# Kernel tuning notes

Measured on AMD Instinct MI355X. Metric: run time of the kernel, lower is better.

Reference implementation:

```python
import jax, jax.numpy as jnp
import numpy as np

S, B, I, H, O = 1024, 64, 512, 2048, 512


def setup_inputs() -> dict:
    key = jax.random.key(0)
    k1, k2, k3, k4, k5 = jax.random.split(key, 5)
    X = jax.random.normal(k1, (S, B, I), dtype=jnp.float32)
    W_ih = jax.random.normal(k2, (H, I), dtype=jnp.float32) * (1.0 / np.sqrt(I))
    hh = jax.random.uniform(k3, (H,), dtype=jnp.float32)  # clamped-to-[-1,1] diagonal recurrence
    W_ho = jax.random.normal(k4, (O, H), dtype=jnp.float32) * (1.0 / np.sqrt(H))
    b_ho = jax.random.normal(k5, (O,), dtype=jnp.float32) * 0.01
    return {"X": X, "W_ih": W_ih, "hh": hh, "W_ho": W_ho, "b_ho": b_ho}


def reference(X, W_ih, hh, W_ho, b_ho):
    # Batch the input->hidden projection over the whole sequence in one GEMM:
    # u[s,b,h] = X[s,b,i] @ W_ih[h,i]^T
    u = jnp.einsum('sbi,hi->sbh', X, W_ih)
    h0 = jnp.zeros((X.shape[1], W_ih.shape[0]), dtype=X.dtype)

    def step(h, u_t):
        h_new = jnp.abs(u_t + hh * h)
        return h_new, None

    h_final, _ = jax.lax.scan(step, h0, u)
    Y = h_final @ W_ho.T + b_ho  # [B, O]
    return Y
```

## Files before the change

kernel.cpp:

```cpp
#include <hip/hip_runtime.h>
#include <hip/hip_bf16.h>
#include <stdint.h>

#define S_LEN 1024
#define B_SZ  64
#define I_SZ  512
#define H_SZ  2048
#define O_SZ  512
#define BH    (B_SZ * H_SZ)

typedef __bf16  bf16x8 __attribute__((ext_vector_type(8)));
typedef float   f32x4  __attribute__((ext_vector_type(4)));

static __device__ __forceinline__ ushort f2bf(float f) {
  union { float f; unsigned u; } v; v.f = f;
  unsigned r = v.u + 0x7FFFu + ((v.u >> 16) & 1u);
  return (ushort)(r >> 16);
}

#define GLOAD_LDS16(gp, lp) \
  __builtin_amdgcn_global_load_lds( \
      (__attribute__((address_space(1))) void*)(gp), \
      (__attribute__((address_space(3))) void*)(lp), 16, 0, 0)

__global__ __launch_bounds__(256) void convert_f32_bf16_kernel(
    const float4* __restrict__ in, ushort4* __restrict__ out, int n4) {
  int i = blockIdx.x * 256 + threadIdx.x;
  if (i >= n4) return;
  float4 v = in[i];
  ushort4 o; o.x = f2bf(v.x); o.y = f2bf(v.y); o.z = f2bf(v.z); o.w = f2bf(v.w);
  out[i] = o;
}

__global__ __launch_bounds__(256, 2) void gemm_u_kernel(
    const ushort* __restrict__ A, const ushort* __restrict__ Bm,
    ushort* __restrict__ U) {
  __shared__ __align__(16) ushort smem[17408];
  ushort* As = smem;
  ushort* Bs = smem + 8192;

  const int tid  = threadIdx.x;
  const int wave = tid >> 6;
  const int lane = tid & 63;

  const int b  = blockIdx.x;
  const int x  = b & 7;
  const int j  = b >> 3;
  const int bn = j & 15;
  const int bm = ((j >> 4) << 3) | x;

  const int wm = (wave >> 1) * 64;
  const int wn = (wave & 1) * 64;
  const int ml = lane & 15;
  const int q  = lane >> 4;

  f32x4 acc[4][4] = {};

  const int r0     = wave * 32;
  const int srow   = lane >> 3;
  const int schunk = ((lane & 7) - srow) & 7;
  const ushort* gA = A  + (size_t)(bm * 128 + r0 + srow) * I_SZ + schunk * 8;
  const ushort* gB = Bm + (size_t)(bn * 128 + r0 + srow) * I_SZ + schunk * 8;
  ushort* lA = As + r0 * 64;
  ushort* lB = Bs + r0 * 64;

  int swz[2];
  swz[0] = ((q + ml) & 7) * 8;
  swz[1] = ((4 + q + ml) & 7) * 8;
  int arow[4], brow[4];
  #pragma unroll
  for (int i = 0; i < 4; ++i) {
    arow[i] = (wm + i * 16 + ml) * 64;
    brow[i] = (wn + i * 16 + ml) * 64;
  }

  for (int kt = 0; kt < I_SZ / 64; ++kt) {
    __syncthreads();
    #pragma unroll
    for (int jj = 0; jj < 4; ++jj) {
      GLOAD_LDS16(gA + (size_t)(jj * 8) * I_SZ + kt * 64, lA + jj * 512);
      GLOAD_LDS16(gB + (size_t)(jj * 8) * I_SZ + kt * 64, lB + jj * 512);
    }
    __syncthreads();
    #pragma unroll
    for (int ks = 0; ks < 2; ++ks) {
      bf16x8 af[4], bfr[4];
      #pragma unroll
      for (int i = 0; i < 4; ++i) {
        af[i]  = *(const bf16x8*)&As[arow[i] + swz[ks]];
        bfr[i] = *(const bf16x8*)&Bs[brow[i] + swz[ks]];
      }
      #pragma unroll
      for (int mi = 0; mi < 4; ++mi)
        #pragma unroll
        for (int ni = 0; ni < 4; ++ni)
          acc[mi][ni] = __builtin_amdgcn_mfma_f32_16x16x32_bf16(
              af[mi], bfr[ni], acc[mi][ni], 0, 0, 0);
    }
  }

  __syncthreads();
  ushort* Cs = smem;
  const int rl0 = wm + q * 4;
  #pragma unroll
  for (int mi = 0; mi < 4; ++mi)
    #pragma unroll
    for (int ni = 0; ni < 4; ++ni)
      #pragma unroll
      for (int r = 0; r < 4; ++r)
        Cs[(rl0 + mi * 16 + r) * 136 + wn + ni * 16 + ml] = f2bf(acc[mi][ni][r]);
  __syncthreads();

  const size_t gbase = (size_t)(bm * 128) * H_SZ + bn * 128;
  #pragma unroll
  for (int i = 0; i < 8; ++i) {
    int chunk = i * 256 + tid;
    int row = chunk >> 4, c8 = chunk & 15;
    uint4 v = *(const uint4*)&Cs[row * 136 + c8 * 8];
    *(uint4*)&U[gbase + (size_t)row * H_SZ + c8 * 8] = v;
  }
}

__global__ __launch_bounds__(256) void scan_kernel(
    const uint* __restrict__ U2, const float* __restrict__ hh,
    float* __restrict__ hstate) {
  int p = blockIdx.x * 256 + threadIdx.x;
  int h0 = (2 * p) & (H_SZ - 1);
  float c0 = hh[h0], c1 = hh[h0 + 1];
  float ha = 0.0f, hb = 0.0f;
  const uint* Up = U2 + p;
  for (int s0 = 0; s0 < S_LEN; s0 += 16) {
    uint v[16];
    #pragma unroll
    for (int t = 0; t < 16; ++t) v[t] = Up[(size_t)(s0 + t) * (BH / 2)];
    #pragma unroll
    for (int t = 0; t < 16; ++t) {
      float ua = __builtin_bit_cast(float, (v[t] & 0xffffu) << 16);
      float ub = __builtin_bit_cast(float, v[t] & 0xffff0000u);
      ha = fabsf(ua + c0 * ha);
      hb = fabsf(ub + c1 * hb);
    }
  }
  ((float2*)hstate)[p] = make_float2(ha, hb);
}

__global__ __launch_bounds__(256) void init_y_kernel(
    const float* __restrict__ bho, float* __restrict__ Y) {
  int idx = blockIdx.x * 256 + threadIdx.x;
  Y[idx] = bho[idx & (O_SZ - 1)];
}

__global__ __launch_bounds__(256) void final_tiled_kernel(
    const float* __restrict__ hstate, const float* __restrict__ Who,
    float* __restrict__ Y) {
  __shared__ float Ws[64 * 68];
  __shared__ float Hs[64 * 68];
  const int tid = threadIdx.x;
  const int og = blockIdx.x, kc = blockIdx.y;
  const int to = tid & 15, tb = tid >> 4;
  float acc[4][4] = {};
  #pragma unroll
  for (int ks = 0; ks < 2; ++ks) {
    const int k0 = kc * 128 + ks * 64;
    const int r = tid >> 2, cg = (tid & 3) * 16;
    #pragma unroll
    for (int i2 = 0; i2 < 4; ++i2) {
      *(float4*)&Ws[r * 68 + cg + i2 * 4] =
          *(const float4*)&Who[(size_t)(og * 64 + r) * H_SZ + k0 + cg + i2 * 4];
      *(float4*)&Hs[r * 68 + cg + i2 * 4] =
          *(const float4*)&hstate[(size_t)r * H_SZ + k0 + cg + i2 * 4];
    }
    __syncthreads();
    #pragma unroll 4
    for (int k = 0; k < 64; ++k) {
      float wv[4], hv[4];
      #pragma unroll
      for (int jj2 = 0; jj2 < 4; ++jj2) wv[jj2] = Ws[(to * 4 + jj2) * 68 + k];
      #pragma unroll
      for (int ii = 0; ii < 4; ++ii) hv[ii] = Hs[(tb * 4 + ii) * 68 + k];
      #pragma unroll
      for (int ii = 0; ii < 4; ++ii)
        #pragma unroll
        for (int jj2 = 0; jj2 < 4; ++jj2)
          acc[ii][jj2] += hv[ii] * wv[jj2];
    }
    __syncthreads();
  }
  #pragma unroll
  for (int ii = 0; ii < 4; ++ii)
    #pragma unroll
    for (int jj2 = 0; jj2 < 4; ++jj2)
      atomicAdd(&Y[(size_t)(tb * 4 + ii) * O_SZ + og * 64 + to * 4 + jj2],
                acc[ii][jj2]);
}

extern "C" void kernel_launch(void* const* d_in, const int* in_sizes, int n_in,
                              void* d_out, int out_size, void* d_ws, size_t ws_size,
                              hipStream_t stream) {
  (void)in_sizes; (void)n_in; (void)out_size; (void)ws_size;
  const float* X   = (const float*)d_in[0];
  const float* Wih = (const float*)d_in[1];
  const float* hh  = (const float*)d_in[2];
  const float* Who = (const float*)d_in[3];
  const float* bho = (const float*)d_in[4];
  float* Y = (float*)d_out;

  const size_t XBF = (size_t)S_LEN * B_SZ * I_SZ * 2;
  const size_t WBF = (size_t)H_SZ * I_SZ * 2;
  const size_t HST = (size_t)BH * 4;

  char* w = (char*)d_ws;
  ushort* Xbf    = (ushort*)w;
  ushort* Wbf    = (ushort*)(w + XBF);
  float*  hstate = (float*) (w + XBF + WBF);
  ushort* U      = (ushort*)(w + XBF + WBF + HST);

  {
    int n4x = (int)((size_t)S_LEN * B_SZ * I_SZ / 4);
    convert_f32_bf16_kernel<<<n4x / 256, 256, 0, stream>>>(
        (const float4*)X, (ushort4*)Xbf, n4x);
    int n4w = (int)((size_t)H_SZ * I_SZ / 4);
    convert_f32_bf16_kernel<<<n4w / 256, 256, 0, stream>>>(
        (const float4*)Wih, (ushort4*)Wbf, n4w);
  }

  gemm_u_kernel<<<8192, 256, 0, stream>>>(Xbf, Wbf, U);

  scan_kernel<<<(BH / 2) / 256, 256, 0, stream>>>((const uint*)U, hh, hstate);

  init_y_kernel<<<(B_SZ * O_SZ) / 256, 256, 0, stream>>>(bho, Y);
  final_tiled_kernel<<<dim3(O_SZ / 64, 16), 256, 0, stream>>>(hstate, Who, Y);
}
```

Before: 453.3 us.

## Fuse input projection GEMM with diagonal recurrence scan per batch/hidden tile

Each block now owns one batch element and one 128-wide hidden slice. It walks the sequence in 128-step chunks, computing the projection tile with MFMA and scanning it from LDS, so the large bf16 U intermediate is never written to or read from global memory. The separate scan kernel and the U workspace are removed. The trade-off is that each chunk's scan runs serially on only 128 threads between GEMM phases. The block now loads X rows strided across the sequence, and occupancy rises to 4 blocks per CU to hide that serial section.

```diff
diff --git a/kernel.cpp b/kernel.cpp
--- a/kernel.cpp
+++ b/kernel.cpp
@@ -16,6 +16,9 @@
   union { float f; unsigned u; } v; v.f = f;
   unsigned r = v.u + 0x7FFFu + ((v.u >> 16) & 1u);
   return (ushort)(r >> 16);
+}
+static __device__ __forceinline__ float bf2f(ushort u) {
+  return __builtin_bit_cast(float, (unsigned)u << 16);
 }
 
 #define GLOAD_LDS16(gp, lp) \
@@ -32,35 +35,36 @@
   out[i] = o;
 }
 
-__global__ __launch_bounds__(256, 2) void gemm_u_kernel(
-    const ushort* __restrict__ A, const ushort* __restrict__ Bm,
-    ushort* __restrict__ U) {
-  __shared__ __align__(16) ushort smem[17408];
+__global__ __launch_bounds__(256, 4) void fused_gemm_scan_kernel(
+    const ushort* __restrict__ Xbf,
+    const ushort* __restrict__ Wbf,
+    const float* __restrict__ hh,
+    float* __restrict__ hstate) {
+  __shared__ __align__(16) ushort smem[16896];
   ushort* As = smem;
   ushort* Bs = smem + 8192;
+  ushort* Cs = smem;
 
   const int tid  = threadIdx.x;
   const int wave = tid >> 6;
   const int lane = tid & 63;
 
-  const int b  = blockIdx.x;
-  const int x  = b & 7;
-  const int j  = b >> 3;
-  const int bn = j & 15;
-  const int bm = ((j >> 4) << 3) | x;
+  const int bid = blockIdx.x;
+  const int x = bid & 7;
+  const int g = bid >> 3;
+  const int b  = (x << 3) | (g & 7);
+  const int ht = g >> 3;
 
   const int wm = (wave >> 1) * 64;
   const int wn = (wave & 1) * 64;
   const int ml = lane & 15;
   const int q  = lane >> 4;
 
-  f32x4 acc[4][4] = {};
-
   const int r0     = wave * 32;
   const int srow   = lane >> 3;
   const int schunk = ((lane & 7) - srow) & 7;
-  const ushort* gA = A  + (size_t)(bm * 128 + r0 + srow) * I_SZ + schunk * 8;
-  const ushort* gB = Bm + (size_t)(bn * 128 + r0 + srow) * I_SZ + schunk * 8;
+  const ushort* gA0 = Xbf + ((size_t)(r0 + srow) * B_SZ + b) * I_SZ + schunk * 8;
+  const ushort* gB  = Wbf + (size_t)(ht * 128 + r0 + srow) * I_SZ + schunk * 8;
   ushort* lA = As + r0 * 64;
   ushort* lB = Bs + r0 * 64;
 
@@ -74,74 +78,62 @@
     brow[i] = (wn + i * 16 + ml) * 64;
   }
 
-  for (int kt = 0; kt < I_SZ / 64; ++kt) {
-    __syncthreads();
+  float c = 0.0f, hst = 0.0f;
+  if (tid < 128) c = hh[ht * 128 + tid];
+
+  for (int st = 0; st < 8; ++st) {
+    f32x4 acc[4][4] = {};
+    const ushort* gA = gA0 + (size_t)st * 128 * B_SZ * I_SZ;
+
+    for (int kt = 0; kt < I_SZ / 64; ++kt) {
+      __syncthreads();
+      #pragma unroll
+      for (int jj = 0; jj < 4; ++jj) {
+        GLOAD_LDS16(gA + (size_t)(jj * 8) * B_SZ * I_SZ + kt * 64, lA + jj * 512);
+        GLOAD_LDS16(gB + (size_t)(jj * 8) * I_SZ + kt * 64, lB + jj * 512);
+      }
+      __syncthreads();
+      #pragma unroll
+      for (int ks = 0; ks < 2; ++ks) {
+        bf16x8 af[4], bfr[4];
+        #pragma unroll
+        for (int i = 0; i < 4; ++i) {
+          af[i]  = *(const bf16x8*)&As[arow[i] + swz[ks]];
+          bfr[i] = *(const bf16x8*)&Bs[brow[i] + swz[ks]];
+        }
+        #pragma unroll
+        for (int mi = 0; mi < 4; ++mi)
+          #pragma unroll
+          for (int ni = 0; ni < 4; ++ni)
+            acc[mi][ni] = __builtin_amdgcn_mfma_f32_16x16x32_bf16(
+                af[mi], bfr[ni], acc[mi][ni], 0, 0, 0);
+      }
+    }
+
+    __syncthreads();
+    const int rl0 = wm + q * 4;
     #pragma unroll
-    for (int jj = 0; jj < 4; ++jj) {
-      GLOAD_LDS16(gA + (size_t)(jj * 8) * I_SZ + kt * 64, lA + jj * 512);
-      GLOAD_LDS16(gB + (size_t)(jj * 8) * I_SZ + kt * 64, lB + jj * 512);
-    }
-    __syncthreads();
-    #pragma unroll
-    for (int ks = 0; ks < 2; ++ks) {
-      bf16x8 af[4], bfr[4];
-      #pragma unroll
-      for (int i = 0; i < 4; ++i) {
-        af[i]  = *(const bf16x8*)&As[arow[i] + swz[ks]];
-        bfr[i] = *(const bf16x8*)&Bs[brow[i] + swz[ks]];
+    for (int mi = 0; mi < 4; ++mi)
+      #pragma unroll
+      for (int ni = 0; ni < 4; ++ni)
+        #pragma unroll
+        for (int r = 0; r < 4; ++r)
+          Cs[(rl0 + mi * 16 + r) * 132 + wn + ni * 16 + ml] = f2bf(acc[mi][ni][r]);
+    __syncthreads();
+
+    if (tid < 128) {
+      #pragma unroll
+      for (int s8 = 0; s8 < 128; s8 += 8) {
+        float uv[8];
+        #pragma unroll
+        for (int t = 0; t < 8; ++t) uv[t] = bf2f(Cs[(s8 + t) * 132 + tid]);
+        #pragma unroll
+        for (int t = 0; t < 8; ++t) hst = fabsf(uv[t] + c * hst);
       }
-      #pragma unroll
-      for (int mi = 0; mi < 4; ++mi)
-        #pragma unroll
-        for (int ni = 0; ni < 4; ++ni)
-          acc[mi][ni] = __builtin_amdgcn_mfma_f32_16x16x32_bf16(
-              af[mi], bfr[ni], acc[mi][ni], 0, 0, 0);
-    }
-  }
-
-  __syncthreads();
-  ushort* Cs = smem;
-  const int rl0 = wm + q * 4;
-  #pragma unroll
-  for (int mi = 0; mi < 4; ++mi)
-    #pragma unroll
-    for (int ni = 0; ni < 4; ++ni)
-      #pragma unroll
-      for (int r = 0; r < 4; ++r)
-        Cs[(rl0 + mi * 16 + r) * 136 + wn + ni * 16 + ml] = f2bf(acc[mi][ni][r]);
-  __syncthreads();
-
-  const size_t gbase = (size_t)(bm * 128) * H_SZ + bn * 128;
-  #pragma unroll
-  for (int i = 0; i < 8; ++i) {
-    int chunk = i * 256 + tid;
-    int row = chunk >> 4, c8 = chunk & 15;
-    uint4 v = *(const uint4*)&Cs[row * 136 + c8 * 8];
-    *(uint4*)&U[gbase + (size_t)row * H_SZ + c8 * 8] = v;
-  }
-}
-
-__global__ __launch_bounds__(256) void scan_kernel(
-    const uint* __restrict__ U2, const float* __restrict__ hh,
-    float* __restrict__ hstate) {
-  int p = blockIdx.x * 256 + threadIdx.x;
-  int h0 = (2 * p) & (H_SZ - 1);
-  float c0 = hh[h0], c1 = hh[h0 + 1];
-  float ha = 0.0f, hb = 0.0f;
-  const uint* Up = U2 + p;
-  for (int s0 = 0; s0 < S_LEN; s0 += 16) {
-    uint v[16];
-    #pragma unroll
-    for (int t = 0; t < 16; ++t) v[t] = Up[(size_t)(s0 + t) * (BH / 2)];
-    #pragma unroll
-    for (int t = 0; t < 16; ++t) {
-      float ua = __builtin_bit_cast(float, (v[t] & 0xffffu) << 16);
-      float ub = __builtin_bit_cast(float, v[t] & 0xffff0000u);
-      ha = fabsf(ua + c0 * ha);
-      hb = fabsf(ub + c1 * hb);
-    }
-  }
-  ((float2*)hstate)[p] = make_float2(ha, hb);
+    }
+  }
+
+  if (tid < 128) hstate[(size_t)b * H_SZ + ht * 128 + tid] = hst;
 }
 
 __global__ __launch_bounds__(256) void init_y_kernel(
@@ -207,13 +199,11 @@
 
   const size_t XBF = (size_t)S_LEN * B_SZ * I_SZ * 2;
   const size_t WBF = (size_t)H_SZ * I_SZ * 2;
-  const size_t HST = (size_t)BH * 4;
 
   char* w = (char*)d_ws;
   ushort* Xbf    = (ushort*)w;
   ushort* Wbf    = (ushort*)(w + XBF);
   float*  hstate = (float*) (w + XBF + WBF);
-  ushort* U      = (ushort*)(w + XBF + WBF + HST);
 
   {
     int n4x = (int)((size_t)S_LEN * B_SZ * I_SZ / 4);
@@ -224,9 +214,7 @@
         (const float4*)Wih, (ushort4*)Wbf, n4w);
   }
 
-  gemm_u_kernel<<<8192, 256, 0, stream>>>(Xbf, Wbf, U);
-
-  scan_kernel<<<(BH / 2) / 256, 256, 0, stream>>>((const uint*)U, hh, hstate);
+  fused_gemm_scan_kernel<<<1024, 256, 0, stream>>>(Xbf, Wbf, hh, hstate);
 
   init_y_kernel<<<(B_SZ * O_SZ) / 256, 256, 0, stream>>>(bho, Y);
   final_tiled_kernel<<<dim3(O_SZ / 64, 16), 256, 0, stream>>>(hstate, Who, Y);
```

New measurement: 414.3 us. 8.6% less time.
